# Kernel tuning notes

Hardware: AMD Instinct MI355X
Metric: run time of the kernel (lower is better)

## Reference

```python
import jax, jax.numpy as jnp
import numpy as np

PIXEL_SIZE = 0.1
PI = 3.141592653589793


def setup_inputs() -> dict:
    key = jax.random.key(0)
    batch = jax.random.normal(key, (128, 1, 512, 512), dtype=jnp.float32)
    return {"batch": batch}


def _hann_window(roi):
    # lin = linspace(-roi/2, roi/2, roi); r[i,j] = sqrt(lin[j]^2 + lin[i]^2)
    lin = jnp.linspace(-roi / 2, roi / 2, roi, dtype=jnp.float32)
    r = jnp.sqrt(lin[None, :] ** 2 + lin[:, None] ** 2)
    hann = 0.5 * (1.0 + jnp.cos(PI * r / (roi / 2)))
    hann = jnp.where(r > roi / 2, 0.0, hann)
    return hann  # [roi, roi]


def _radial_segments(roi, n_freq):
    # radialDst = round(sqrt(xx^2 + yy^2)) with x = arange(-cx, roi-cx)
    cx = roi // 2
    x = np.arange(-cx, roi - cx, dtype=np.float64)
    xx, yy = np.meshgrid(x, x, indexing="ij")
    rad = np.round(np.sqrt(xx ** 2 + yy ** 2)).astype(np.int32)
    # bins >= n_freq go into an overflow segment that is discarded
    seg = np.where(rad < n_freq, rad, n_freq)
    return jnp.asarray(seg.ravel())


def reference(batch):
    px = PIXEL_SIZE
    roi = batch.shape[-1]
    cx = roi // 2
    n_freq = cx + 1
    nyquist = 1.0 / (2.0 * px)

    # subtract per-ROI mean
    batch_nm = batch - jnp.mean(batch, axis=(2, 3), keepdims=True)

    # Hann-windowed 2D power spectrum, averaged over realizations
    hann = _hann_window(roi)[None, None, :, :]
    F = jnp.fft.fftshift(jnp.fft.fft2(batch_nm * hann, axes=(2, 3)), axes=(2, 3))
    ps = jnp.mean(jnp.abs(F) ** 2, axis=0)            # [1, roi, roi]
    nps2D = (px ** 2 / roi ** 2) * jnp.squeeze(ps)    # [roi, roi]

    # single-pass radial mean binning (replaces per-k boolean-mask loop)
    seg = _radial_segments(roi, n_freq)
    flat = nps2D.ravel()
    sums = jax.ops.segment_sum(flat, seg, num_segments=n_freq + 1)[:n_freq]
    counts = jax.ops.segment_sum(jnp.ones_like(flat), seg, num_segments=n_freq + 1)[:n_freq]
    nps1D = sums / counts

    f1D = jnp.linspace(0.0, nyquist, n_freq, dtype=jnp.float32)
    return nps1D, nps2D, f1D
```

## Files before the change

### kernel.cpp

```cpp
#include <hip/hip_runtime.h>
#include <hip/hip_fp16.h>

#define N 512
#define NF 257
#define NB 128
#define PI_F 3.14159265358979323846f
#define C_SQ2 0.70710678118654752440f

__device__ __forceinline__ float2 cmul(float2 a, float2 b) {
    return make_float2(a.x * b.x - a.y * b.y, a.x * b.y + a.y * b.x);
}
__device__ __forceinline__ void bf(float2& a, float2& b) {
    float2 t = b;
    b = make_float2(a.x - t.x, a.y - t.y);
    a = make_float2(a.x + t.x, a.y + t.y);
}
__device__ __forceinline__ void bf_tw(float2& a, float2& b, float2 w) {
    float2 t = cmul(b, w);
    b = make_float2(a.x - t.x, a.y - t.y);
    a = make_float2(a.x + t.x, a.y + t.y);
}
__device__ __forceinline__ void bf_ni(float2& a, float2& b) {
    float2 t = make_float2(b.y, -b.x);
    b = make_float2(a.x - t.x, a.y - t.y);
    a = make_float2(a.x + t.x, a.y + t.y);
}
__device__ __forceinline__ void lds_fence() {
    asm volatile("s_waitcnt lgkmcnt(0)" ::: "memory");
}

__device__ __forceinline__ void fft512(float2 v[8], float* lre, float* lim, int l) {
    const float2 w64  = make_float2(C_SQ2, -C_SQ2);
    const float2 w192 = make_float2(-C_SQ2, -C_SQ2);
    bf(v[0], v[1]); bf(v[2], v[3]); bf(v[4], v[5]); bf(v[6], v[7]);
    bf(v[0], v[2]); bf_ni(v[1], v[3]); bf(v[4], v[6]); bf_ni(v[5], v[7]);
    bf(v[0], v[4]); bf_tw(v[1], v[5], w64); bf_ni(v[2], v[6]); bf_tw(v[3], v[7], w192);
#pragma unroll
    for (int e = 0; e < 8; e++) { lre[9 * l + e] = v[e].x; lim[9 * l + e] = v[e].y; }
    lds_fence();
    int g = l >> 3, r = l & 7;
#pragma unroll
    for (int t = 0; t < 8; t++) {
        int p = 72 * g + 9 * t + r;
        v[t].x = lre[p]; v[t].y = lim[p];
    }
    float sn, cs;
    __sincosf(-(PI_F / 32.0f) * (float)r, &sn, &cs);
    float2 W1 = make_float2(cs, sn);
    float2 W2 = cmul(W1, W1);
    float2 W3 = cmul(W2, W2);
    float2 W2n = make_float2(W2.y, -W2.x);
    bf_tw(v[0], v[1], W3); bf_tw(v[2], v[3], W3); bf_tw(v[4], v[5], W3); bf_tw(v[6], v[7], W3);
    bf_tw(v[0], v[2], W2); bf_tw(v[1], v[3], W2n); bf_tw(v[4], v[6], W2); bf_tw(v[5], v[7], W2n);
    {
        float2 W1a = cmul(W1, w64);
        float2 W1n = make_float2(W1.y, -W1.x);
        float2 W1c = cmul(W1, w192);
        bf_tw(v[0], v[4], W1); bf_tw(v[1], v[5], W1a); bf_tw(v[2], v[6], W1n); bf_tw(v[3], v[7], W1c);
    }
#pragma unroll
    for (int t = 0; t < 8; t++) {
        int p = 72 * g + 9 * t + r;
        lre[p] = v[t].x; lim[p] = v[t].y;
    }
    lds_fence();
#pragma unroll
    for (int t = 0; t < 8; t++) {
        int p = 72 * t + l + (l >> 3);
        v[t].x = lre[p]; v[t].y = lim[p];
    }
    __sincosf(-(PI_F / 256.0f) * (float)l, &sn, &cs);
    float2 Wc = make_float2(cs, sn);
    float2 w2 = cmul(Wc, Wc);
    float2 w4 = cmul(w2, w2);
    float2 w2n = make_float2(w2.y, -w2.x);
    bf_tw(v[0], v[1], w4); bf_tw(v[2], v[3], w4); bf_tw(v[4], v[5], w4); bf_tw(v[6], v[7], w4);
    bf_tw(v[0], v[2], w2); bf_tw(v[1], v[3], w2n); bf_tw(v[4], v[6], w2); bf_tw(v[5], v[7], w2n);
    {
        float2 Wca = cmul(Wc, w64);
        float2 Wcn = make_float2(Wc.y, -Wc.x);
        float2 Wcc = cmul(Wc, w192);
        bf_tw(v[0], v[4], Wc); bf_tw(v[1], v[5], Wca); bf_tw(v[2], v[6], Wcn); bf_tw(v[3], v[7], Wcc);
    }
}

__global__ void zero_kernel(float* __restrict__ acc, float* __restrict__ bins,
                            float* __restrict__ meanacc) {
    int i = blockIdx.x * blockDim.x + threadIdx.x;
    if (i < N * N) acc[i] = 0.0f;
    if (i < 2 * (NF + 1)) bins[i] = 0.0f;
    if (i < NB) meanacc[i] = 0.0f;
}

__global__ __launch_bounds__(256) void hanntab_kernel(float* __restrict__ htab) {
    int i = blockIdx.x * 256 + threadIdx.x;
    int r = i >> 9, c = i & (N - 1);
    const float step = (float)N / (float)(N - 1);
    float a = -0.5f * (float)N + (float)r * step;
    float b = -0.5f * (float)N + (float)c * step;
    float rr = sqrtf(a * a + b * b);
    float h = (rr > 256.0f) ? 0.0f : 0.5f * (1.0f + cosf(rr * (PI_F / 256.0f)));
    htab[i] = h;
}

__global__ __launch_bounds__(512) void hannfft_kernel(const float* __restrict__ htab,
                                                      float2* __restrict__ Hrow) {
    __shared__ float sm[9216];
    int tid = threadIdx.x;
    int w = tid >> 6, l = tid & 63;
    int rowbase = blockIdx.x << 4;
    int r1 = rowbase + 2 * w, r2 = r1 + 1;
    const float* h1row = htab + (size_t)r1 * N;
    const float* h2row = htab + (size_t)r2 * N;

    float2 v[8];
    int rl = __brev((unsigned)l) >> 26;
#pragma unroll
    for (int e = 0; e < 8; e++) {
        int src = (int)((__brev((unsigned)e) >> 29) << 6) + rl;
        v[e].x = h1row[src];
        v[e].y = h2row[src];
    }

    float* lre = sm + w * 1152;
    float* lim = lre + 576;
    fft512(v, lre, lim, l);
    __syncthreads();

    float* tre = sm;
    float* tim = sm + 4240;
    int lr0 = 2 * w, lr1 = lr0 + 1;
    int sl = (64 - l) & 63;
#pragma unroll
    for (int t = 0; t <= 4; t++) {
        float2 a = v[7 - t];
        float zfx = __shfl(a.x, sl);
        float zfy = __shfl(a.y, sl);
        if (l == 0) { float2 o = v[(8 - t) & 7]; zfx = o.x; zfy = o.y; }
        float2 z = v[t];
        int col = 64 * t + l;
        if (col < NF) {
            tre[lr0 * 265 + col] = 0.5f * (z.x + zfx);
            tim[lr0 * 265 + col] = 0.5f * (z.y - zfy);
            tre[lr1 * 265 + col] = 0.5f * (z.y + zfy);
            tim[lr1 * 265 + col] = 0.5f * (zfx - z.x);
        }
    }
    __syncthreads();

    int c0 = tid >> 4, rr = tid & 15;
#pragma unroll
    for (int it = 0; it < 9; it++) {
        int c = it * 32 + c0;
        if (c < NF) {
            float2 val = make_float2(tre[rr * 265 + c], tim[rr * 265 + c]);
            Hrow[(size_t)c * N + rowbase + rr] = val;
        }
    }
}

__global__ __launch_bounds__(512) void rowfft_kernel(const float* __restrict__ x,
                                                     const float* __restrict__ htab,
                                                     float* __restrict__ meanacc,
                                                     __half2* __restrict__ inter) {
    __shared__ float sm[9216];
    __shared__ float redsum[8];
    int tid = threadIdx.x;
    int w = tid >> 6, l = tid & 63;
    int img = blockIdx.x >> 5;
    int rowbase = (blockIdx.x & 31) << 4;
    int r1 = rowbase + 2 * w, r2 = r1 + 1;
    const float* x1 = x + ((size_t)img * N + r1) * N;
    const float* x2 = x1 + N;
    const float* h1row = htab + (size_t)r1 * N;
    const float* h2row = htab + (size_t)r2 * N;

    float2 v[8];
    float rsum = 0.0f;
    int rl = __brev((unsigned)l) >> 26;
#pragma unroll
    for (int e = 0; e < 8; e++) {
        int src = (int)((__brev((unsigned)e) >> 29) << 6) + rl;
        float xv1 = x1[src], xv2 = x2[src];
        rsum += xv1 + xv2;
        v[e].x = xv1 * h1row[src];
        v[e].y = xv2 * h2row[src];
    }
#pragma unroll
    for (int off = 32; off > 0; off >>= 1) rsum += __shfl_down(rsum, off);
    if (l == 0) redsum[w] = rsum;

    float* lre = sm + w * 1152;
    float* lim = lre + 576;
    fft512(v, lre, lim, l);
    __syncthreads();
    if (tid == 0) {
        float s = 0.0f;
#pragma unroll
        for (int i = 0; i < 8; i++) s += redsum[i];
        atomicAdd(meanacc + img, s);
    }

    __half2* tile = (__half2*)sm;
    int lr0 = 2 * w, lr1 = lr0 + 1;
    int sl = (64 - l) & 63;
#pragma unroll
    for (int t = 0; t <= 4; t++) {
        float2 a = v[7 - t];
        float zfx = __shfl(a.x, sl);
        float zfy = __shfl(a.y, sl);
        if (l == 0) { float2 o = v[(8 - t) & 7]; zfx = o.x; zfy = o.y; }
        float2 z = v[t];
        int col = 64 * t + l;
        if (col < NF) {
            tile[lr0 * 265 + col] = __floats2half2_rn(0.5f * (z.x + zfx), 0.5f * (z.y - zfy));
            tile[lr1 * 265 + col] = __floats2half2_rn(0.5f * (z.y + zfy), 0.5f * (zfx - z.x));
        }
    }
    __syncthreads();

    int c0 = tid >> 4, rr = tid & 15;
#pragma unroll
    for (int it = 0; it < 9; it++) {
        int c = it * 32 + c0;
        if (c < NF) {
            inter[((size_t)img * NF + c) * N + rowbase + rr] = tile[rr * 265 + c];
        }
    }
}

__global__ __launch_bounds__(256) void colfft_kernel(const __half2* __restrict__ inter,
                                                     const float2* __restrict__ Hrow,
                                                     const float* __restrict__ meanacc,
                                                     float* __restrict__ accT) {
    __shared__ float sm[4608];
    int tid = threadIdx.x;
    int w = tid >> 6, l = tid & 63;
    int col = blockIdx.x * 4 + w;
    int colc = col < NF ? col : NF - 1;
    int b0 = blockIdx.y * 8;
    float* lre = sm + w * 1152;
    float* lim = lre + 576;
    int rl = __brev((unsigned)l) >> 26;

    int off[8];
#pragma unroll
    for (int e = 0; e < 8; e++)
        off[e] = (int)((__brev((unsigned)e) >> 29) << 6) + rl;

    float2 hv[8];
    const float2* hbase = Hrow + (size_t)colc * N;
#pragma unroll
    for (int e = 0; e < 8; e++) hv[e] = hbase[off[e]];

    float pw[8];
#pragma unroll
    for (int t = 0; t < 8; t++) pw[t] = 0.0f;

    __half2 nv[8];
    const __half2* base0 = inter + ((size_t)b0 * NF + colc) * N;
#pragma unroll
    for (int e = 0; e < 8; e++) nv[e] = base0[off[e]];

    for (int bi = 0; bi < 8; bi++) {
        float mn = meanacc[b0 + bi] * (1.0f / ((float)N * (float)N));
        float2 v[8];
#pragma unroll
        for (int e = 0; e < 8; e++) {
            float2 z = __half22float2(nv[e]);
            v[e] = make_float2(z.x - mn * hv[e].x, z.y - mn * hv[e].y);
        }
        if (bi < 7) {
            const __half2* nb = inter + ((size_t)(b0 + bi + 1) * NF + colc) * N;
#pragma unroll
            for (int e = 0; e < 8; e++) nv[e] = nb[off[e]];
        }
        fft512(v, lre, lim, l);
#pragma unroll
        for (int t = 0; t < 8; t++)
            pw[t] += v[t].x * v[t].x + v[t].y * v[t].y;
    }

    if (col < NF) {
        int sv = (col + 256) & 511;
#pragma unroll
        for (int t = 0; t < 8; t++) {
            int k = 64 * t + l;
            int su = (k + 256) & 511;
            atomicAdd(&accT[(size_t)sv * N + su], pw[t]);
        }
        if (col >= 1 && col <= 255) {
            int sv2 = (768 - col) & 511;
#pragma unroll
            for (int t = 0; t < 8; t++) {
                int k = 64 * t + l;
                int su2 = (768 - k) & 511;
                atomicAdd(&accT[(size_t)sv2 * N + su2], pw[t]);
            }
        }
    }
}

__global__ __launch_bounds__(256) void finalize2d_kernel(const float* __restrict__ accT,
                                                         float* __restrict__ out2d,
                                                         float* __restrict__ bins) {
    __shared__ float lsum[NF];
    __shared__ float lcnt[NF];
    int t = threadIdx.x;
    for (int i = t; i < NF; i += 256) { lsum[i] = 0.0f; lcnt[i] = 0.0f; }
    __syncthreads();
    const float scale = (0.1f * 0.1f) / ((float)N * (float)N) / (float)NB;
    int idx = blockIdx.x * 256 + t;
    int stride = gridDim.x * 256;
    for (int q = idx; q < N * N; q += stride) {
        int j = q >> 9, i = q & (N - 1);
        float v = accT[q] * scale;
        out2d[(size_t)i * N + j] = v;
        float xi = (float)(i - N / 2), yj = (float)(j - N / 2);
        int rad = (int)rintf(sqrtf(xi * xi + yj * yj));
        if (rad < NF) {
            atomicAdd(&lsum[rad], v);
            atomicAdd(&lcnt[rad], 1.0f);
        }
    }
    __syncthreads();
    for (int i = t; i < NF; i += 256) {
        if (lsum[i] != 0.0f || lcnt[i] != 0.0f) {
            atomicAdd(&bins[i], lsum[i]);
            atomicAdd(&bins[NF + 1 + i], lcnt[i]);
        }
    }
}

__global__ void finalize1d_kernel(const float* __restrict__ bins, float* __restrict__ out) {
    int t = blockIdx.x * blockDim.x + threadIdx.x;
    if (t < NF) {
        out[t] = bins[t] / bins[NF + 1 + t];
        out[NF + N * N + t] = (float)t * (5.0f / 256.0f);
    }
}

extern "C" void kernel_launch(void* const* d_in, const int* in_sizes, int n_in,
                              void* d_out, int out_size, void* d_ws, size_t ws_size,
                              hipStream_t stream) {
    const float* x = (const float*)d_in[0];
    float* out = (float*)d_out;
    char* ws = (char*)d_ws;

    float* accT    = (float*)ws;
    float* meanacc = (float*)(ws + (size_t)N * N * sizeof(float));
    float* bins    = meanacc + NB;
    size_t off_h = (size_t)N * N * sizeof(float) + NB * sizeof(float)
                   + 2 * (NF + 1) * sizeof(float);
    off_h = (off_h + 255) & ~(size_t)255;
    float2* Hrow = (float2*)(ws + off_h);
    size_t off_t = off_h + (size_t)NF * N * sizeof(float2);
    off_t = (off_t + 255) & ~(size_t)255;
    float* htab = (float*)(ws + off_t);
    size_t off_inter = off_t + (size_t)N * N * sizeof(float);
    off_inter = (off_inter + 255) & ~(size_t)255;
    __half2* inter = (__half2*)(ws + off_inter);

    zero_kernel<<<dim3((N * N + 255) / 256), dim3(256), 0, stream>>>(accT, bins, meanacc);
    hanntab_kernel<<<dim3(N * N / 256), dim3(256), 0, stream>>>(htab);
    hannfft_kernel<<<dim3(32), dim3(512), 0, stream>>>(htab, Hrow);
    rowfft_kernel<<<dim3(NB * 32), dim3(512), 0, stream>>>(x, htab, meanacc, inter);
    colfft_kernel<<<dim3(65, 16), dim3(256), 0, stream>>>(inter, Hrow, meanacc, accT);
    finalize2d_kernel<<<dim3(256), dim3(256), 0, stream>>>(accT, out + NF, bins);
    finalize1d_kernel<<<dim3(2), dim3(256), 0, stream>>>(bins, out);
}
```

Before: 270.4 us.

## Vectorize FFT input loads with LDS bit-reverse and halve power accumulator atomics

Row and column FFT kernels now load contiguous float4 chunks and perform the bit-reversal permutation through an extra LDS pass, instead of issuing strided scalar gathers. LDS staging switches from split re/im float arrays to interleaved float2. The column kernel now accumulates power into a half-spectrum buffer with one set of atomics, and the finalize kernel expands Hermitian symmetry when writing the fftshifted output. This trades an extra LDS round trip per FFT for coalesced global loads and roughly half the global atomics.

```diff
diff --git a/kernel.cpp b/kernel.cpp
--- a/kernel.cpp
+++ b/kernel.cpp
@@ -29,21 +29,18 @@
     asm volatile("s_waitcnt lgkmcnt(0)" ::: "memory");
 }
 
-__device__ __forceinline__ void fft512(float2 v[8], float* lre, float* lim, int l) {
+__device__ __forceinline__ void fft512_core(float2 v[8], float2* st, int l) {
     const float2 w64  = make_float2(C_SQ2, -C_SQ2);
     const float2 w192 = make_float2(-C_SQ2, -C_SQ2);
     bf(v[0], v[1]); bf(v[2], v[3]); bf(v[4], v[5]); bf(v[6], v[7]);
     bf(v[0], v[2]); bf_ni(v[1], v[3]); bf(v[4], v[6]); bf_ni(v[5], v[7]);
     bf(v[0], v[4]); bf_tw(v[1], v[5], w64); bf_ni(v[2], v[6]); bf_tw(v[3], v[7], w192);
 #pragma unroll
-    for (int e = 0; e < 8; e++) { lre[9 * l + e] = v[e].x; lim[9 * l + e] = v[e].y; }
+    for (int e = 0; e < 8; e++) st[9 * l + e] = v[e];
     lds_fence();
     int g = l >> 3, r = l & 7;
 #pragma unroll
-    for (int t = 0; t < 8; t++) {
-        int p = 72 * g + 9 * t + r;
-        v[t].x = lre[p]; v[t].y = lim[p];
-    }
+    for (int t = 0; t < 8; t++) v[t] = st[72 * g + 9 * t + r];
     float sn, cs;
     __sincosf(-(PI_F / 32.0f) * (float)r, &sn, &cs);
     float2 W1 = make_float2(cs, sn);
@@ -59,16 +56,10 @@
         bf_tw(v[0], v[4], W1); bf_tw(v[1], v[5], W1a); bf_tw(v[2], v[6], W1n); bf_tw(v[3], v[7], W1c);
     }
 #pragma unroll
-    for (int t = 0; t < 8; t++) {
-        int p = 72 * g + 9 * t + r;
-        lre[p] = v[t].x; lim[p] = v[t].y;
-    }
+    for (int t = 0; t < 8; t++) st[72 * g + 9 * t + r] = v[t];
     lds_fence();
 #pragma unroll
-    for (int t = 0; t < 8; t++) {
-        int p = 72 * t + l + (l >> 3);
-        v[t].x = lre[p]; v[t].y = lim[p];
-    }
+    for (int t = 0; t < 8; t++) v[t] = st[72 * t + l + (l >> 3)];
     __sincosf(-(PI_F / 256.0f) * (float)l, &sn, &cs);
     float2 Wc = make_float2(cs, sn);
     float2 w2 = cmul(Wc, Wc);
@@ -84,10 +75,22 @@
     }
 }
 
-__global__ void zero_kernel(float* __restrict__ acc, float* __restrict__ bins,
+__device__ __forceinline__ void fft512_nat(float2 v[8], float2* st, int l) {
+#pragma unroll
+    for (int e = 0; e < 8; e++) st[9 * l + e] = v[e];
+    lds_fence();
+    int rl = __brev((unsigned)l) >> 26;
+    int rp = rl + (rl >> 3);
+    const int bre[8] = {0, 4, 2, 6, 1, 5, 3, 7};
+#pragma unroll
+    for (int e = 0; e < 8; e++) v[e] = st[72 * bre[e] + rp];
+    fft512_core(v, st, l);
+}
+
+__global__ void zero_kernel(float* __restrict__ accH, float* __restrict__ bins,
                             float* __restrict__ meanacc) {
     int i = blockIdx.x * blockDim.x + threadIdx.x;
-    if (i < N * N) acc[i] = 0.0f;
+    if (i < NF * N) accH[i] = 0.0f;
     if (i < 2 * (NF + 1)) bins[i] = 0.0f;
     if (i < NB) meanacc[i] = 0.0f;
 }
@@ -110,21 +113,18 @@
     int w = tid >> 6, l = tid & 63;
     int rowbase = blockIdx.x << 4;
     int r1 = rowbase + 2 * w, r2 = r1 + 1;
-    const float* h1row = htab + (size_t)r1 * N;
-    const float* h2row = htab + (size_t)r2 * N;
+    const float4* h1 = (const float4*)(htab + (size_t)r1 * N) + 2 * l;
+    const float4* h2 = (const float4*)(htab + (size_t)r2 * N) + 2 * l;
+    float4 ha = h1[0], hb = h1[1], hc = h2[0], hd = h2[1];
 
     float2 v[8];
-    int rl = __brev((unsigned)l) >> 26;
-#pragma unroll
-    for (int e = 0; e < 8; e++) {
-        int src = (int)((__brev((unsigned)e) >> 29) << 6) + rl;
-        v[e].x = h1row[src];
-        v[e].y = h2row[src];
-    }
-
-    float* lre = sm + w * 1152;
-    float* lim = lre + 576;
-    fft512(v, lre, lim, l);
+    v[0] = make_float2(ha.x, hc.x); v[1] = make_float2(ha.y, hc.y);
+    v[2] = make_float2(ha.z, hc.z); v[3] = make_float2(ha.w, hc.w);
+    v[4] = make_float2(hb.x, hd.x); v[5] = make_float2(hb.y, hd.y);
+    v[6] = make_float2(hb.z, hd.z); v[7] = make_float2(hb.w, hd.w);
+
+    float2* st = (float2*)sm + w * 576;
+    fft512_nat(v, st, l);
     __syncthreads();
 
     float* tre = sm;
@@ -170,29 +170,33 @@
     int img = blockIdx.x >> 5;
     int rowbase = (blockIdx.x & 31) << 4;
     int r1 = rowbase + 2 * w, r2 = r1 + 1;
-    const float* x1 = x + ((size_t)img * N + r1) * N;
-    const float* x2 = x1 + N;
-    const float* h1row = htab + (size_t)r1 * N;
-    const float* h2row = htab + (size_t)r2 * N;
+    const float4* x1 = (const float4*)(x + ((size_t)img * N + r1) * N) + 2 * l;
+    const float4* x2 = (const float4*)(x + ((size_t)img * N + r2) * N) + 2 * l;
+    const float4* h1 = (const float4*)(htab + (size_t)r1 * N) + 2 * l;
+    const float4* h2 = (const float4*)(htab + (size_t)r2 * N) + 2 * l;
+
+    float4 xa = x1[0], xb = x1[1], xc = x2[0], xd = x2[1];
+    float4 ha = h1[0], hb = h1[1], hc = h2[0], hd = h2[1];
+
+    float rsum = ((xa.x + xa.y) + (xa.z + xa.w)) + ((xb.x + xb.y) + (xb.z + xb.w))
+               + ((xc.x + xc.y) + (xc.z + xc.w)) + ((xd.x + xd.y) + (xd.z + xd.w));
 
     float2 v[8];
-    float rsum = 0.0f;
-    int rl = __brev((unsigned)l) >> 26;
-#pragma unroll
-    for (int e = 0; e < 8; e++) {
-        int src = (int)((__brev((unsigned)e) >> 29) << 6) + rl;
-        float xv1 = x1[src], xv2 = x2[src];
-        rsum += xv1 + xv2;
-        v[e].x = xv1 * h1row[src];
-        v[e].y = xv2 * h2row[src];
-    }
+    v[0] = make_float2(xa.x * ha.x, xc.x * hc.x);
+    v[1] = make_float2(xa.y * ha.y, xc.y * hc.y);
+    v[2] = make_float2(xa.z * ha.z, xc.z * hc.z);
+    v[3] = make_float2(xa.w * ha.w, xc.w * hc.w);
+    v[4] = make_float2(xb.x * hb.x, xd.x * hd.x);
+    v[5] = make_float2(xb.y * hb.y, xd.y * hd.y);
+    v[6] = make_float2(xb.z * hb.z, xd.z * hd.z);
+    v[7] = make_float2(xb.w * hb.w, xd.w * hd.w);
+
 #pragma unroll
     for (int off = 32; off > 0; off >>= 1) rsum += __shfl_down(rsum, off);
     if (l == 0) redsum[w] = rsum;
 
-    float* lre = sm + w * 1152;
-    float* lim = lre + 576;
-    fft512(v, lre, lim, l);
+    float2* st = (float2*)sm + w * 576;
+    fft512_nat(v, st, l);
     __syncthreads();
     if (tid == 0) {
         float s = 0.0f;
@@ -232,76 +236,60 @@
 __global__ __launch_bounds__(256) void colfft_kernel(const __half2* __restrict__ inter,
                                                      const float2* __restrict__ Hrow,
                                                      const float* __restrict__ meanacc,
-                                                     float* __restrict__ accT) {
+                                                     float* __restrict__ accH) {
     __shared__ float sm[4608];
     int tid = threadIdx.x;
     int w = tid >> 6, l = tid & 63;
     int col = blockIdx.x * 4 + w;
     int colc = col < NF ? col : NF - 1;
     int b0 = blockIdx.y * 8;
-    float* lre = sm + w * 1152;
-    float* lim = lre + 576;
-    int rl = __brev((unsigned)l) >> 26;
-
-    int off[8];
-#pragma unroll
-    for (int e = 0; e < 8; e++)
-        off[e] = (int)((__brev((unsigned)e) >> 29) << 6) + rl;
-
-    float2 hv[8];
-    const float2* hbase = Hrow + (size_t)colc * N;
-#pragma unroll
-    for (int e = 0; e < 8; e++) hv[e] = hbase[off[e]];
+    float2* st = (float2*)sm + w * 576;
+
+    union F4F2 { float4 f[4]; float2 c[8]; } hu;
+    const float4* hp = (const float4*)(Hrow + (size_t)colc * N + 8 * l);
+#pragma unroll
+    for (int q = 0; q < 4; q++) hu.f[q] = hp[q];
 
     float pw[8];
 #pragma unroll
     for (int t = 0; t < 8; t++) pw[t] = 0.0f;
 
-    __half2 nv[8];
-    const __half2* base0 = inter + ((size_t)b0 * NF + colc) * N;
-#pragma unroll
-    for (int e = 0; e < 8; e++) nv[e] = base0[off[e]];
+    union F4H { float4 f; __half2 h[4]; };
+    F4H na, nb;
+    const float4* p0 = (const float4*)(inter + ((size_t)b0 * NF + colc) * N + 8 * l);
+    na.f = p0[0]; nb.f = p0[1];
 
     for (int bi = 0; bi < 8; bi++) {
         float mn = meanacc[b0 + bi] * (1.0f / ((float)N * (float)N));
         float2 v[8];
 #pragma unroll
-        for (int e = 0; e < 8; e++) {
-            float2 z = __half22float2(nv[e]);
-            v[e] = make_float2(z.x - mn * hv[e].x, z.y - mn * hv[e].y);
+        for (int e = 0; e < 4; e++) {
+            float2 z = __half22float2(na.h[e]);
+            v[e] = make_float2(z.x - mn * hu.c[e].x, z.y - mn * hu.c[e].y);
+        }
+#pragma unroll
+        for (int e = 0; e < 4; e++) {
+            float2 z = __half22float2(nb.h[e]);
+            v[4 + e] = make_float2(z.x - mn * hu.c[4 + e].x, z.y - mn * hu.c[4 + e].y);
         }
         if (bi < 7) {
-            const __half2* nb = inter + ((size_t)(b0 + bi + 1) * NF + colc) * N;
-#pragma unroll
-            for (int e = 0; e < 8; e++) nv[e] = nb[off[e]];
-        }
-        fft512(v, lre, lim, l);
+            const float4* np = (const float4*)(inter + ((size_t)(b0 + bi + 1) * NF + colc) * N + 8 * l);
+            na.f = np[0]; nb.f = np[1];
+        }
+        fft512_nat(v, st, l);
 #pragma unroll
         for (int t = 0; t < 8; t++)
             pw[t] += v[t].x * v[t].x + v[t].y * v[t].y;
     }
 
     if (col < NF) {
-        int sv = (col + 256) & 511;
-#pragma unroll
-        for (int t = 0; t < 8; t++) {
-            int k = 64 * t + l;
-            int su = (k + 256) & 511;
-            atomicAdd(&accT[(size_t)sv * N + su], pw[t]);
-        }
-        if (col >= 1 && col <= 255) {
-            int sv2 = (768 - col) & 511;
-#pragma unroll
-            for (int t = 0; t < 8; t++) {
-                int k = 64 * t + l;
-                int su2 = (768 - k) & 511;
-                atomicAdd(&accT[(size_t)sv2 * N + su2], pw[t]);
-            }
-        }
-    }
-}
-
-__global__ __launch_bounds__(256) void finalize2d_kernel(const float* __restrict__ accT,
+#pragma unroll
+        for (int t = 0; t < 8; t++)
+            atomicAdd(&accH[(size_t)col * N + 64 * t + l], pw[t]);
+    }
+}
+
+__global__ __launch_bounds__(256) void finalize2d_kernel(const float* __restrict__ accH,
                                                          float* __restrict__ out2d,
                                                          float* __restrict__ bins) {
     __shared__ float lsum[NF];
@@ -312,15 +300,20 @@
     const float scale = (0.1f * 0.1f) / ((float)N * (float)N) / (float)NB;
     int idx = blockIdx.x * 256 + t;
     int stride = gridDim.x * 256;
-    for (int q = idx; q < N * N; q += stride) {
-        int j = q >> 9, i = q & (N - 1);
-        float v = accT[q] * scale;
-        out2d[(size_t)i * N + j] = v;
-        float xi = (float)(i - N / 2), yj = (float)(j - N / 2);
+    for (int q = idx; q < NF * N; q += stride) {
+        int col = q >> 9, k = q & (N - 1);
+        float v = accH[q] * scale;
+        int i1 = (k + 256) & 511, j1 = (col + 256) & 511;
+        out2d[(size_t)i1 * N + j1] = v;
+        float xi = (float)(i1 - 256), yj = (float)(j1 - 256);
         int rad = (int)rintf(sqrtf(xi * xi + yj * yj));
-        if (rad < NF) {
-            atomicAdd(&lsum[rad], v);
-            atomicAdd(&lcnt[rad], 1.0f);
+        if (rad < NF) { atomicAdd(&lsum[rad], v); atomicAdd(&lcnt[rad], 1.0f); }
+        if (col >= 1 && col <= 255) {
+            int i2 = (256 - k) & 511, j2 = (256 - col) & 511;
+            out2d[(size_t)i2 * N + j2] = v;
+            float xi2 = (float)(i2 - 256), yj2 = (float)(j2 - 256);
+            int rad2 = (int)rintf(sqrtf(xi2 * xi2 + yj2 * yj2));
+            if (rad2 < NF) { atomicAdd(&lsum[rad2], v); atomicAdd(&lcnt[rad2], 1.0f); }
         }
     }
     __syncthreads();
@@ -347,10 +340,10 @@
     float* out = (float*)d_out;
     char* ws = (char*)d_ws;
 
-    float* accT    = (float*)ws;
-    float* meanacc = (float*)(ws + (size_t)N * N * sizeof(float));
+    float* accH    = (float*)ws;
+    float* meanacc = (float*)(ws + (size_t)NF * N * sizeof(float));
     float* bins    = meanacc + NB;
-    size_t off_h = (size_t)N * N * sizeof(float) + NB * sizeof(float)
+    size_t off_h = (size_t)NF * N * sizeof(float) + NB * sizeof(float)
                    + 2 * (NF + 1) * sizeof(float);
     off_h = (off_h + 255) & ~(size_t)255;
     float2* Hrow = (float2*)(ws + off_h);
@@ -361,11 +354,11 @@
     off_inter = (off_inter + 255) & ~(size_t)255;
     __half2* inter = (__half2*)(ws + off_inter);
 
-    zero_kernel<<<dim3((N * N + 255) / 256), dim3(256), 0, stream>>>(accT, bins, meanacc);
+    zero_kernel<<<dim3((NF * N + 255) / 256), dim3(256), 0, stream>>>(accH, bins, meanacc);
     hanntab_kernel<<<dim3(N * N / 256), dim3(256), 0, stream>>>(htab);
     hannfft_kernel<<<dim3(32), dim3(512), 0, stream>>>(htab, Hrow);
     rowfft_kernel<<<dim3(NB * 32), dim3(512), 0, stream>>>(x, htab, meanacc, inter);
-    colfft_kernel<<<dim3(65, 16), dim3(256), 0, stream>>>(inter, Hrow, meanacc, accT);
-    finalize2d_kernel<<<dim3(256), dim3(256), 0, stream>>>(accT, out + NF, bins);
+    colfft_kernel<<<dim3(65, 16), dim3(256), 0, stream>>>(inter, Hrow, meanacc, accH);
+    finalize2d_kernel<<<dim3(256), dim3(256), 0, stream>>>(accH, out + NF, bins);
     finalize1d_kernel<<<dim3(2), dim3(256), 0, stream>>>(bins, out);
 }
```

After: 259.0 us. 4.2% less time.
